# Kernel optimization log

Measured on AMD Instinct MI355X. Metric: run time of the kernel, lower is better.

The kernel has to match this reference:

```python
import jax, jax.numpy as jnp
import numpy as np

NR, NS, TAU, GW = 32, 64, 0.1, 0.5
NEG = jnp.float32(-1e30)

def _nrm(x):
    return x / jnp.maximum(jnp.linalg.norm(x, axis=-1, keepdims=True), 1e-12)

def _pair_loss(fb, ub, am, nm, ra, rp, rn):
    # fb [HW,D] features, ub [HW] uncertainty, am/nm [HW] bool anchor(=pos)/neg masks,
    # ra/rp/rn [HW] uniform random scores standing in for torch.randperm.
    def sel(mask, r, k):  # random subset of size k from mask (invalid slots flagged)
        _, idx = jax.lax.top_k(jnp.where(mask, r, NEG), k)
        return idx, mask[idx]
    def hard(mask, r):  # randperm[:2*Ns] then topk Ns by uncertainty
        cidx, cval = sel(mask, r, 2 * NS)
        _, t = jax.lax.top_k(jnp.where(cval, ub[cidx], NEG), NS)
        return cidx[t], cval[t]
    aidx, aval = sel(am, ra, NR)
    pidx, pval = hard(am, rp)
    nidx, nval = hard(nm, rn)
    q  = _nrm(fb[aidx])   # [NR,D]
    P  = _nrm(fb[pidx])   # [NS,D]
    Ng = _nrm(fb[nidx])   # [NS,D]
    pw = pval.astype(fb.dtype)[:, None]
    nw = nval.astype(fb.dtype)[:, None]
    p = (jnp.exp(P @ q.T / TAU) * pw).sum(0)   # [NR]
    n = (jnp.exp(Ng @ q.T / TAU) * nw).sum(0)  # [NR]
    inc = (am.sum() >= 1) & (nm.sum() >= 1)
    p = p + (1.0 - inc.astype(p.dtype))  # safe when excluded
    per = -jnp.log(p / (p + n + 1e-8))
    af = aval.astype(per.dtype)
    bl = (per * af).sum() / jnp.maximum(af.sum(), 1.0)
    return jnp.where(inc, bl, 0.0), inc

def _forward(feat, labels, prob_ori, prob_aug, unc, r_anc, r_pos, r_neg,
             w1, b1, gamma, beta, w2, b2):
    B, D, H, W = feat.shape
    # proj: 1x1 conv -> BN (training stats) -> relu -> 1x1 conv
    x = jnp.einsum('bdhw,ed->behw', feat, w1) + b1[None, :, None, None]
    mu = x.mean((0, 2, 3), keepdims=True)
    var = x.var((0, 2, 3), keepdims=True)
    x = gamma[None, :, None, None] * (x - mu) / jnp.sqrt(var + 1e-5) + beta[None, :, None, None]
    x = jax.nn.relu(x)
    proj = jnp.einsum('bdhw,ed->behw', x, w2) + b2[None, :, None, None]

    rel = prob_ori.argmax(1) == prob_aug.argmax(1)
    diff = unc > 0.5
    valid = (rel & diff).reshape(B, -1)
    lab = labels.reshape(B, -1)
    f = proj.transpose(0, 2, 3, 1).reshape(B, -1, D)
    uf = unc.reshape(B, -1)
    m1 = valid & (lab == 1)
    m0 = valid & (lab == 0)

    # ---- local loss: classes (1 vs 0) and (0 vs 1) ----
    anc = jnp.stack([m1, m0], 1)  # [B,2,HW]
    neg = jnp.stack([m0, m1], 1)
    pair = jax.vmap(jax.vmap(_pair_loss, in_axes=(None, None, 0, 0, 0, 0, 0)),
                    in_axes=(0, 0, 0, 0, 0, 0, 0))
    bl, inc = pair(f, uf, anc, neg, r_anc, r_pos, r_neg)
    l_local = bl.sum() / jnp.maximum(inc.sum(), 1)

    # ---- global loss with sequential memory bank (bank starts empty) ----
    fgf = m1.astype(f.dtype); bgf = m0.astype(f.dtype)
    cf = fgf.sum(1); cb = bgf.sum(1)
    m_fg = (f * fgf[..., None]).sum(1) / jnp.maximum(cf, 1.0)[:, None]
    m_bg = (f * bgf[..., None]).sum(1) / jnp.maximum(cb, 1.0)[:, None]
    vg = (cf >= 1) & (cb >= 1)
    qf, qb = _nrm(m_fg), _nrm(m_bg)
    # bank content at step b: prototypes of valid j <= b (detached)
    M = ((jnp.arange(B)[None, :] <= jnp.arange(B)[:, None]) & vg[None, :]).astype(f.dtype)  # [b,j]
    Sf = jnp.exp(jax.lax.stop_gradient(qb) @ qf.T / TAU)  # [j,b]
    Sb = jnp.exp(jax.lax.stop_gradient(qf) @ qb.T / TAU)
    nf = jnp.einsum('jb,bj->b', Sf, M)
    nb = jnp.einsum('jb,bj->b', Sb, M)
    pf = jnp.exp((qf * qf).sum(-1) / TAU)
    pb = jnp.exp((qb * qb).sum(-1) / TAU)
    lg = -jnp.log(pf / (pf + nf + 1e-8)) - jnp.log(pb / (pb + nb + 1e-8))
    l_global = (vg.astype(f.dtype) * lg).sum() / jnp.maximum(vg.sum(), 1)

    return l_local + GW * l_global, l_local, l_global

def setup_inputs() -> dict:
    key = jax.random.key(0)
    ks = jax.random.split(key, 16)
    B, D, H, W = 4, 256, 128, 128
    HW = H * W
    return {
        'feat': jax.random.normal(ks[0], (B, D, H, W), jnp.float32),
        'labels': jax.random.randint(ks[1], (B, H, W), 0, 2, jnp.int32),
        'prob_ori': jax.random.uniform(ks[2], (B, 2, H, W), jnp.float32),
        'prob_aug': jax.random.uniform(ks[3], (B, 2, H, W), jnp.float32),
        'unc': jax.random.uniform(ks[4], (B, H, W), jnp.float32),
        'r_anc': jax.random.uniform(ks[5], (B, 2, HW), jnp.float32),
        'r_pos': jax.random.uniform(ks[6], (B, 2, HW), jnp.float32),
        'r_neg': jax.random.uniform(ks[7], (B, 2, HW), jnp.float32),
        'w1': jax.random.normal(ks[8], (D, D), jnp.float32) * 0.05,
        'b1': jnp.zeros((D,), jnp.float32),
        'gamma': jnp.ones((D,), jnp.float32),
        'beta': jnp.zeros((D,), jnp.float32),
        'w2': jax.random.normal(ks[9], (D, D), jnp.float32) * 0.05,
        'b2': jnp.zeros((D,), jnp.float32),
    }

def reference(feat, labels, prob_ori, prob_aug, unc, r_anc, r_pos, r_neg,
              w1, b1, gamma, beta, w2, b2):
    return _forward(feat, labels, prob_ori, prob_aug, unc, r_anc, r_pos, r_neg,
                    w1, b1, gamma, beta, w2, b2)
```

## Files before the change

### kernel.cpp

```cpp
#include <hip/hip_runtime.h>
#include <hip/hip_bf16.h>
#include <float.h>
#include <math.h>

#define HW 16384
#define NBATCH 4
#define DIM 256
#define NEGV (-1e30f)
#define NPP 160

#define OFF_CHAN_SUM 0
#define OFF_CHAN_SQ  1024
#define OFF_MEAN     2048
#define OFF_ISTD     3072
#define OFF_S1       4096
#define OFF_S0       8192
#define OFF_CF       12288
#define OFF_CB       12304
#define OFF_BL       12320
#define OFF_INCF     12352
#define OFF_PPCNT    12416
#define OFF_QBUF     16384
#define OFF_BCNT     24576
#define OFF_MCLS     40960
#define OFF_SELIDX   303104
#define OFF_SELW     308224
#define OFF_ROWS     313344
#define OFF_W1T      1624064
#define OFF_RAW      1886208
#define OFF_CKEYS_XL 68995072
#define WS_NEED_FAST 68995072ull
#define WS_NEED_XL   72140800ull

#define NSEL 24

__device__ __forceinline__ unsigned f2mono(float f) {
  unsigned u = __float_as_uint(f);
  return (u & 0x80000000u) ? ~u : (u | 0x80000000u);
}

__device__ __forceinline__ void sort_desc(unsigned long long* sk, int* si, int n, int tid) {
  for (int ksz = 2; ksz <= n; ksz <<= 1) {
    for (int j = ksz >> 1; j > 0; j >>= 1) {
      __syncthreads();
      if (tid < n) {
        int ixj = tid ^ j;
        if (ixj > tid) {
          unsigned long long a = sk[tid], b = sk[ixj];
          bool up = (tid & ksz) == 0;
          if (up ? (a < b) : (a > b)) {
            sk[tid] = b; sk[ixj] = a;
            int t2 = si[tid]; si[tid] = si[ixj]; si[ixj] = t2;
          }
        }
      }
    }
  }
  __syncthreads();
}

__global__ __launch_bounds__(256) void k_maskc2(
    const float* __restrict__ po, const float* __restrict__ pa,
    const float* __restrict__ unc, const int* __restrict__ lab,
    const float* __restrict__ r_anc, const float* __restrict__ r_pos,
    const float* __restrict__ r_neg, const float* __restrict__ w1,
    int* __restrict__ mcls, int* __restrict__ bcnt,
    unsigned long long* __restrict__ ckeys, float* __restrict__ w1T,
    float* __restrict__ chanSum, float* __restrict__ chanSq,
    float* __restrict__ S1, float* __restrict__ S0,
    int* __restrict__ ppcnt) {
  __shared__ int lcnt[24];
  int tid = threadIdx.x;
  int g = blockIdx.x * 256 + tid;
  int b = g >> 14;
  int lb = blockIdx.x & 63;
  int i = g & (HW - 1);
  if (tid < 24) lcnt[tid] = 0;
  __syncthreads();
  float o0 = po[(size_t)(b*2+0)*HW + i];
  float o1 = po[(size_t)(b*2+1)*HW + i];
  float a0 = pa[(size_t)(b*2+0)*HW + i];
  float a1 = pa[(size_t)(b*2+1)*HW + i];
  bool rel = ((o1 > o0) == (a1 > a0));
  bool valid = rel && (unc[g] > 0.5f);
  int l = lab[g];
  int cls = valid ? ((l == 1) ? 1 : 2) : 0;
  mcls[g] = cls;
  int t0 = 0, t1 = 0, t2 = 0, loc0 = 0, loc1 = 0, loc2 = 0;
  unsigned long long k0 = 0, k1 = 0, k2 = 0;
  if (cls) {
    int co = cls - 1;
    unsigned idxf = (unsigned)(16383 - i);
    t0 = (b*2 + co)*3 + 0;
    t1 = (b*2 + co)*3 + 1;
    t2 = (b*2 + (1 - co))*3 + 2;
    k0 = ((unsigned long long)f2mono(r_anc[(size_t)(b*2 + co)*HW + i]) << 14) | idxf;
    k1 = ((unsigned long long)f2mono(r_pos[(size_t)(b*2 + co)*HW + i]) << 14) | idxf;
    k2 = ((unsigned long long)f2mono(r_neg[(size_t)(b*2 + (1 - co))*HW + i]) << 14) | idxf;
    loc0 = atomicAdd(&lcnt[t0], 1);
    loc1 = atomicAdd(&lcnt[t1], 1);
    loc2 = atomicAdd(&lcnt[t2], 1);
  }
  __syncthreads();
  if (tid < 24 && (tid / 6) == b)
    bcnt[tid*64 + lb] = lcnt[tid];
  if (cls) {
    ckeys[(size_t)t0*HW + lb*256 + loc0] = k0;
    ckeys[(size_t)t1*HW + lb*256 + loc1] = k1;
    ckeys[(size_t)t2*HW + lb*256 + loc2] = k2;
  }
  if (blockIdx.x < 16) {
    int d0 = blockIdx.x * 16;
    float v[16];
    #pragma unroll
    for (int j = 0; j < 16; ++j) v[j] = w1[(size_t)tid*DIM + d0 + j];
    #pragma unroll
    for (int j = 0; j < 16; ++j) w1T[(size_t)(d0 + j)*DIM + tid] = v[j];
  }
  if (blockIdx.x == 16) { chanSum[tid] = 0.f; chanSq[tid] = 0.f; }
  if (blockIdx.x == 17) {
    #pragma unroll
    for (int j = 0; j < 4; ++j) S1[j*256 + tid] = 0.f;
  }
  if (blockIdx.x == 18) {
    #pragma unroll
    for (int j = 0; j < 4; ++j) S0[j*256 + tid] = 0.f;
  }
  if (blockIdx.x == 19 && tid == 0) *ppcnt = 0;
}

__device__ void selc_body(const int* __restrict__ bcnt,
                          const unsigned long long* __restrict__ ckeys,
                          const float* __restrict__ unc,
                          int* __restrict__ selIdx, float* __restrict__ selW,
                          int* __restrict__ cf, int* __restrict__ cb,
                          int task, int tid, char* sh) {
  unsigned long long* sk = (unsigned long long*)sh;
  int* si    = (int*)(sh + 1024);
  int* cIdx  = (int*)(sh + 1536);
  int* hist  = (int*)(sh + 2048);
  int* sufs  = (int*)(sh + 3072);
  int* sbcnt = (int*)(sh + 4096);
  unsigned char* cVal = (unsigned char*)(sh + 4352);
  int* scal  = (int*)(sh + 4480);

  int pair = task / 3, which = task % 3;
  int b = pair >> 1, c = pair & 1;
  const unsigned long long* keys = ckeys + (size_t)task * HW;
  if (tid < 64) sbcnt[tid] = bcnt[task*64 + tid];
  __syncthreads();
  if (tid == 0) { int s = 0; for (int i2 = 0; i2 < 64; ++i2) s += sbcnt[i2]; scal[3] = s; }
  __syncthreads();
  int cnt = scal[3];
  if (which == 0 && tid == 0) { if (c == 0) cf[b] = cnt; else cb[b] = cnt; }
  int K1 = (which == 0) ? 32 : 128;
  int outBase = pair*NPP + (which == 0 ? 0 : (which == 1 ? 32 : 96));

  int mseg = tid >> 2;
  int msub = tid & 3;
  int mcnt = sbcnt[mseg];
  const unsigned long long* mkeys = keys + mseg*256;

  unsigned long long pref = 0;
  if (cnt > K1) {
    const int shifts[6]  = {38, 30, 22, 14, 6, 0};
    const int bitsArr[6] = { 8,  8,  8,  8, 8, 6};
    int k = K1;
    for (int p = 0; p < 6; ++p) {
      int shift = shifts[p], nbits = bitsArr[p], nb = 1 << nbits;
      hist[tid] = 0;
      __syncthreads();
      for (int pos = msub; pos < mcnt; pos += 4) {
        unsigned long long key = mkeys[pos];
        if ((key >> (shift + nbits)) == pref)
          atomicAdd(&hist[(int)((key >> shift) & (nb - 1))], 1);
      }
      __syncthreads();
      if (tid < nb) sufs[tid] = hist[tid];
      __syncthreads();
      for (int off = 1; off < nb; off <<= 1) {
        int add = 0;
        if (tid < nb && tid + off < nb) add = sufs[tid + off];
        __syncthreads();
        if (tid < nb) sufs[tid] += add;
        __syncthreads();
      }
      if (tid < nb) {
        int sthis = sufs[tid];
        int snext = (tid + 1 < nb) ? sufs[tid + 1] : 0;
        if (sthis >= k && snext < k) { scal[0] = tid; scal[1] = k - snext; }
      }
      __syncthreads();
      pref = (pref << nbits) | (unsigned)scal[0];
      k = scal[1];
      __syncthreads();
    }
  }

  if (tid == 0) scal[2] = 0;
  __syncthreads();
  for (int pos = msub; pos < mcnt; pos += 4) {
    unsigned long long key = mkeys[pos];
    if (key >= pref) {
      int p2 = atomicAdd(&scal[2], 1);
      if (p2 < 128) { sk[p2] = key; si[p2] = 16383 - (int)(key & 16383); }
    }
  }
  __syncthreads();
  int gcnt = scal[2];
  if (tid < K1 && tid >= gcnt) { sk[tid] = 0ull; si[tid] = 0; }

  sort_desc(sk, si, K1, tid);

  if (which == 0) {
    if (tid < 32) {
      selIdx[outBase + tid] = si[tid];
      selW[outBase + tid]   = (sk[tid] != 0ull) ? 1.f : 0.f;
    }
    return;
  }

  if (tid < 128) {
    cIdx[tid] = si[tid];
    cVal[tid] = (sk[tid] != 0ull) ? 1 : 0;
  }
  __syncthreads();
  if (tid < 128) {
    float u2 = cVal[tid] ? unc[(size_t)b*HW + cIdx[tid]] : NEGV;
    sk[tid] = ((unsigned long long)f2mono(u2) << 7) | (unsigned)(127 - tid);
    si[tid] = tid;
  }
  sort_desc(sk, si, 128, tid);
  if (tid < 64) {
    int t = si[tid];
    selIdx[outBase + tid] = cIdx[t];
    selW[outBase + tid]   = cVal[t] ? 1.f : 0.f;
  }
}

__global__ __launch_bounds__(256) void k_selc2(
    const int* __restrict__ bcnt, const unsigned long long* __restrict__ ckeys,
    const float* __restrict__ unc,
    int* __restrict__ selIdx, float* __restrict__ selW,
    int* __restrict__ cf, int* __restrict__ cb) {
  __shared__ __align__(16) char sh[4608];
  selc_body(bcnt, ckeys, unc, selIdx, selW, cf, cb, blockIdx.x, threadIdx.x, sh);
}

#define BK 32
#define LDA 128

__device__ void mm8_body(
    const float* __restrict__ feat, const float* __restrict__ w1T,
    const int* __restrict__ mcls,
    float* __restrict__ chanSum, float* __restrict__ chanSq,
    float* __restrict__ rawout, int bid, int tid, float* smem) {
  float* As = smem;
  float* Bs = smem + BK*LDA;
  int ct = bid & 1;
  int rt = bid >> 1;
  int b  = rt >> 7;
  int i0 = (rt & 127) << 7;
  int c0 = ct << 7;
  int tx = tid & 15, ty = tid >> 4;
  float acc[8][8];
  #pragma unroll
  for (int r = 0; r < 8; ++r)
    #pragma unroll
    for (int c = 0; c < 8; ++c) acc[r][c] = 0.f;

  for (int kc = 0; kc < 8; ++kc) {
    int d0 = kc * BK;
    #pragma unroll
    for (int it = 0; it < 4; ++it) {
      int e = it*1024 + tid*4;
      int k = e >> 7, r = e & 127;
      float4 v = *(const float4*)&feat[((size_t)(b*DIM + d0 + k))*HW + i0 + r];
      *(float4*)&As[k*LDA + r] = v;
    }
    #pragma unroll
    for (int it = 0; it < 4; ++it) {
      int e = it*1024 + tid*4;
      int k = e >> 7, c = e & 127;
      float4 v = *(const float4*)&w1T[(size_t)(d0 + k)*DIM + c0 + c];
      *(float4*)&Bs[k*LDA + c] = v;
    }
    __syncthreads();
    #pragma unroll
    for (int k = 0; k < BK; ++k) {
      float4 a0 = *(const float4*)&As[k*LDA + ty*4];
      float4 a1 = *(const float4*)&As[k*LDA + 64 + ty*4];
      float4 b0 = *(const float4*)&Bs[k*LDA + tx*4];
      float4 b1 = *(const float4*)&Bs[k*LDA + 64 + tx*4];
      float ar[8] = {a0.x,a0.y,a0.z,a0.w, a1.x,a1.y,a1.z,a1.w};
      float bc[8] = {b0.x,b0.y,b0.z,b0.w, b1.x,b1.y,b1.z,b1.w};
      #pragma unroll
      for (int r = 0; r < 8; ++r)
        #pragma unroll
        for (int c = 0; c < 8; ++c)
          acc[r][c] += ar[r]*bc[c];
    }
    __syncthreads();
  }

  float* pS = smem;
  float* pQ = smem + 2048;
  #pragma unroll
  for (int c = 0; c < 8; ++c) {
    int lcol = (c < 4) ? (tx*4 + c) : (64 + tx*4 + (c - 4));
    float s = 0.f, q = 0.f;
    #pragma unroll
    for (int r = 0; r < 8; ++r) { float v = acc[r][c]; s += v; q += v*v; }
    pS[ty*128 + lcol] = s;
    pQ[ty*128 + lcol] = q;
  }
  __syncthreads();
  if (tid < 128) {
    float s = 0.f, q = 0.f;
    #pragma unroll
    for (int t2 = 0; t2 < 16; ++t2) { s += pS[t2*128 + tid]; q += pQ[t2*128 + tid]; }
    atomicAdd(&chanSum[c0 + tid], s);
    atomicAdd(&chanSq[c0 + tid],  q);
  }

  #pragma unroll
  for (int r = 0; r < 8; ++r) {
    int lrow = (r < 4) ? (ty*4 + r) : (64 + ty*4 + (r - 4));
    int g = rt*128 + lrow;
    if (mcls[g] != 0) {
      float4 lo; lo.x = acc[r][0]; lo.y = acc[r][1]; lo.z = acc[r][2]; lo.w = acc[r][3];
      float4 hi; hi.x = acc[r][4]; hi.y = acc[r][5]; hi.z = acc[r][6]; hi.w = acc[r][7];
      *(float4*)&rawout[(size_t)g*DIM + c0 + tx*4]      = lo;
      *(float4*)&rawout[(size_t)g*DIM + c0 + 64 + tx*4] = hi;
    }
  }
}

__global__ __launch_bounds__(256) void k_mmsel(
    const float* __restrict__ feat, const float* __restrict__ w1T,
    const int* __restrict__ mcls,
    float* __restrict__ chanSum, float* __restrict__ chanSq,
    float* __restrict__ rawout,
    const int* __restrict__ bcnt, const unsigned long long* __restrict__ ckeys,
    const float* __restrict__ unc,
    int* __restrict__ selIdx, float* __restrict__ selW,
    int* __restrict__ cf, int* __restrict__ cb, int nSel) {
  __shared__ __align__(16) float smem[2*BK*LDA];
  int bid = blockIdx.x;
  if (bid < nSel)
    selc_body(bcnt, ckeys, unc, selIdx, selW, cf, cb, bid, threadIdx.x, (char*)smem);
  else
    mm8_body(feat, w1T, mcls, chanSum, chanSq, rawout, bid - nSel, threadIdx.x, smem);
}

__global__ __launch_bounds__(256) void k_post(
    const float* __restrict__ raw, const int* __restrict__ mcls,
    const float* __restrict__ chanSum, const float* __restrict__ chanSq,
    const float* __restrict__ gamma, const float* __restrict__ beta,
    const float* __restrict__ w2, const float* __restrict__ b2,
    const int* __restrict__ selIdx, const float* __restrict__ selW,
    float* __restrict__ S1, float* __restrict__ S0,
    float* __restrict__ rows) {
  __shared__ __align__(16) float sh[2048];
  const float nconst = (float)(NBATCH * HW);
  int tid = threadIdx.x;

  if (blockIdx.x < 256) {
    float* p1 = sh;
    float* p2 = sh + 1024;
    int w = tid >> 6, lane = tid & 63;
    int p0 = blockIdx.x << 8;
    int b = p0 >> 14;
    int ch = lane*4;
    float4 G = *(const float4*)&gamma[ch];
    float4 Bt = *(const float4*)&beta[ch];
    float4 CS = *(const float4*)&chanSum[ch];
    float4 CQ = *(const float4*)&chanSq[ch];
    float m0 = CS.x/nconst, m1 = CS.y/nconst, m2 = CS.z/nconst, m3 = CS.w/nconst;
    float v0 = CQ.x/nconst - m0*m0, v1 = CQ.y/nconst - m1*m1;
    float v2 = CQ.z/nconst - m2*m2, v3 = CQ.w/nconst - m3*m3;
    float i0 = 1.0f/sqrtf(v0 + 1e-5f), i1 = 1.0f/sqrtf(v1 + 1e-5f);
    float i2 = 1.0f/sqrtf(v2 + 1e-5f), i3 = 1.0f/sqrtf(v3 + 1e-5f);
    float A0 = G.x*i0, A1 = G.y*i1, A2 = G.z*i2, A3 = G.w*i3;
    float s1[4] = {0,0,0,0}, s0[4] = {0,0,0,0};
    int g0 = p0 + w*64;
    for (int t = 0; t < 64; ++t) {
      int g = g0 + t;
      int cls = mcls[g];
      if (cls == 0) continue;
      float4 v = *(const float4*)&raw[(size_t)g*DIM + ch];
      float r0 = A0*(v.x - m0) + Bt.x; r0 = r0 > 0.f ? r0 : 0.f;
      float r1 = A1*(v.y - m1) + Bt.y; r1 = r1 > 0.f ? r1 : 0.f;
      float r2 = A2*(v.z - m2) + Bt.z; r2 = r2 > 0.f ? r2 : 0.f;
      float r3 = A3*(v.w - m3) + Bt.w; r3 = r3 > 0.f ? r3 : 0.f;
      if (cls == 1) { s1[0]+=r0; s1[1]+=r1; s1[2]+=r2; s1[3]+=r3; }
      else          { s0[0]+=r0; s0[1]+=r1; s0[2]+=r2; s0[3]+=r3; }
    }
    #pragma unroll
    for (int j = 0; j < 4; ++j) {
      p1[w*256 + ch + j] = s1[j];
      p2[w*256 + ch + j] = s0[j];
    }
    __syncthreads();
    float a = p1[tid] + p1[256+tid] + p1[512+tid] + p1[768+tid];
    float d = p2[tid] + p2[256+tid] + p2[512+tid] + p2[768+tid];
    atomicAdd(&S1[b*DIM + tid], a);
    atomicAdd(&S0[b*DIM + tid], d);
  } else {
    float* rl  = sh;
    float* red = sh + 1024;
    int blk = blockIdx.x - 256;
    int slot0 = blk * 4;
    int pair = slot0 / NPP;
    int b = pair >> 1;
    int e = tid;
    float m = chanSum[e] / nconst;
    float v = chanSq[e] / nconst - m*m;
    float istd = 1.0f / sqrtf(v + 1e-5f);
    float A = gamma[e]*istd;
    float Bt = beta[e];
    bool ok[4];
    #pragma unroll
    for (int s = 0; s < 4; ++s) {
      int slot = slot0 + s;
      ok[s] = (selW[slot] != 0.f);
      float rv = 0.f;
      if (ok[s]) {
        int i = selIdx[slot];
        float acc = raw[((size_t)b*HW + i)*DIM + e];
        float bn = A*(acc - m) + Bt;
        rv = bn > 0.f ? bn : 0.f;
      }
      rl[s*256 + e] = rv;
    }
    __syncthreads();
    float b2e = b2[e];
    float pj[4] = {b2e, b2e, b2e, b2e};
    const float4* w4 = (const float4*)&w2[(size_t)e*DIM];
    #pragma unroll 8
    for (int d4 = 0; d4 < DIM/4; ++d4) {
      float4 w = w4[d4];
      #pragma unroll
      for (int s = 0; s < 4; ++s) {
        float4 a = *(const float4*)&rl[s*256 + d4*4];
        pj[s] += a.x*w.x + a.y*w.y + a.z*w.z + a.w*w.w;
      }
    }
    #pragma unroll
    for (int s = 0; s < 4; ++s) red[s*256 + e] = pj[s]*pj[s];
    __syncthreads();
    for (int off = 128; off > 0; off >>= 1) {
      if (e < off) {
        #pragma unroll
        for (int s = 0; s < 4; ++s) red[s*256 + e] += red[s*256 + e + off];
      }
      __syncthreads();
    }
    #pragma unroll
    for (int s = 0; s < 4; ++s) {
      float sc = 1.f / fmaxf(sqrtf(red[s*256]), 1e-12f);
      rows[(size_t)(slot0 + s)*DIM + e] = ok[s] ? pj[s]*sc : 0.f;
    }
  }
}

__device__ void pair_body(
    const float* __restrict__ rows, const float* __restrict__ selW,
    const int* __restrict__ cf, const int* __restrict__ cb,
    float* __restrict__ BL, float* __restrict__ INCF, int pair, int tid) {
  __shared__ float q[32*257];
  __shared__ float pacc[256], nacc[256];
  __shared__ float red[64];
  int b = pair >> 1, c = pair & 1;
  for (int l = tid; l < 32*DIM; l += 256) {
    int r = l >> 8, d = l & 255;
    q[r*257 + d] = rows[((size_t)pair*NPP + r)*DIM + d];
  }
  __syncthreads();
  int g = tid >> 5, r = tid & 31;
  float ap = 0.f, an = 0.f;
  for (int so = 0; so < 8; ++so) {
    int s = so*8 + g;
    const float* Pr = &rows[((size_t)pair*NPP + 32 + s)*DIM];
    const float* Nr = &rows[((size_t)pair*NPP + 96 + s)*DIM];
    float dp = 0.f, dn = 0.f;
    for (int d = 0; d < DIM; ++d) {
      float qv = q[r*257 + d];
      dp += Pr[d]*qv;
      dn += Nr[d]*qv;
    }
    ap += expf(dp*10.f) * selW[pair*NPP + 32 + s];
    an += expf(dn*10.f) * selW[pair*NPP + 96 + s];
  }
  pacc[tid] = ap; nacc[tid] = an;
  __syncthreads();
  if (tid < 32) {
    float p = 0.f, n = 0.f;
    for (int gg = 0; gg < 8; ++gg) { p += pacc[gg*32 + tid]; n += nacc[gg*32 + tid]; }
    int amC = (c == 0) ? cf[b] : cb[b];
    int nmC = (c == 0) ? cb[b] : cf[b];
    bool inc = (amC >= 1) && (nmC >= 1);
    if (!inc) p += 1.f;
    float per = -logf(p / (p + n + 1e-8f));
    float af = selW[pair*NPP + tid];
    red[tid]      = per*af;
    red[32 + tid] = af;
  }
  __syncthreads();
  if (tid == 0) {
    float s = 0.f, sa = 0.f;
    for (int rr = 0; rr < 32; ++rr) { s += red[rr]; sa += red[32+rr]; }
    int amC = (c == 0) ? cf[b] : cb[b];
    int nmC = (c == 0) ? cb[b] : cf[b];
    bool inc = (amC >= 1) && (nmC >= 1);
    float bl = s / fmaxf(sa, 1.f);
    BL[pair]   = inc ? bl : 0.f;
    INCF[pair] = inc ? 1.f : 0.f;
  }
}

__device__ void proto_body(
    const float* __restrict__ S1, const float* __restrict__ S0,
    const int* __restrict__ cf, const int* __restrict__ cb,
    const float* __restrict__ w2, const float* __restrict__ b2,
    float* __restrict__ qbuf, int idx, int l) {
  int b = idx >> 1, side = idx & 1;
  const float* S = (side == 0) ? &S1[b*DIM] : &S0[b*DIM];
  float cnt = (float)((side == 0) ? cf[b] : cb[b]);
  float m[4]; float n2p = 0.f;
  #pragma unroll
  for (int k = 0; k < 4; ++k) {
    int e = l + 64*k;
    float acc = 0.f;
    const float* w2r = &w2[(size_t)e*DIM];
    for (int d = 0; d < DIM; ++d) acc += S[d]*w2r[d];
    float mv = (acc + cnt*b2[e]) / fmaxf(cnt, 1.f);
    m[k] = mv; n2p += mv*mv;
  }
  #pragma unroll
  for (int off = 32; off > 0; off >>= 1) n2p += __shfl_down(n2p, off, 64);
  float n2 = __shfl(n2p, 0, 64);
  float sc = 1.f / fmaxf(sqrtf(n2), 1e-12f);
  #pragma unroll
  for (int k = 0; k < 4; ++k)
    qbuf[(size_t)(side*4 + b)*DIM + l + 64*k] = m[k]*sc;
}

__device__ void glob_body(
    const float* __restrict__ qbuf,
    const int* __restrict__ cf, const int* __restrict__ cb,
    const float* __restrict__ BL, const float* __restrict__ INCF,
    float* __restrict__ out, int l) {
  float qf[4][4], qb[4][4];
  #pragma unroll
  for (int b = 0; b < 4; ++b)
    #pragma unroll
    for (int k = 0; k < 4; ++k) {
      qf[b][k] = qbuf[(size_t)b*DIM + l + 64*k];
      qb[b][k] = qbuf[(size_t)(4 + b)*DIM + l + 64*k];
    }
  float pd[24];
  #pragma unroll
  for (int j = 0; j < 4; ++j)
    #pragma unroll
    for (int b = 0; b < 4; ++b) {
      float s = 0.f;
      #pragma unroll
      for (int k = 0; k < 4; ++k) s += qb[j][k]*qf[b][k];
      pd[j*4 + b] = s;
    }
  #pragma unroll
  for (int b = 0; b < 4; ++b) {
    float s1 = 0.f, s2 = 0.f;
    #pragma unroll
    for (int k = 0; k < 4; ++k) { s1 += qf[b][k]*qf[b][k]; s2 += qb[b][k]*qb[b][k]; }
    pd[16 + b] = s1; pd[20 + b] = s2;
  }
  #pragma unroll
  for (int t = 0; t < 24; ++t)
    #pragma unroll
    for (int off = 32; off > 0; off >>= 1)
      pd[t] += __shfl_down(pd[t], off, 64);
  if (l == 0) {
    bool vg[4]; float vgs = 0.f;
    for (int b = 0; b < 4; ++b) {
      vg[b] = (cf[b] >= 1) && (cb[b] >= 1);
      if (vg[b]) vgs += 1.f;
    }
    float gsum = 0.f;
    for (int b = 0; b < 4; ++b) {
      float nf = 0.f, nb = 0.f;
      for (int j = 0; j <= b; ++j) if (vg[j]) {
        nf += expf(10.f*pd[j*4 + b]);
        nb += expf(10.f*pd[b*4 + j]);
      }
      float pf = expf(10.f*pd[16 + b]);
      float pb = expf(10.f*pd[20 + b]);
      float lg = -logf(pf/(pf + nf + 1e-8f)) - logf(pb/(pb + nb + 1e-8f));
      if (vg[b]) gsum += lg;
    }
    float l_global = gsum / fmaxf(vgs, 1.f);
    float bls = 0.f, incs = 0.f;
    for (int p = 0; p < 8; ++p) { bls += BL[p]; incs += INCF[p]; }
    float l_local = bls / fmaxf(incs, 1.f);
    out[0] = l_local + 0.5f*l_global;
    out[1] = l_local;
    out[2] = l_global;
  }
}

__global__ __launch_bounds__(256) void k_pp(
    const float* __restrict__ rows, const float* __restrict__ selW,
    const int* __restrict__ cf, const int* __restrict__ cb,
    float* __restrict__ BL, float* __restrict__ INCF,
    const float* __restrict__ S1, const float* __restrict__ S0,
    const float* __restrict__ w2, const float* __restrict__ b2,
    float* __restrict__ qbuf, int* __restrict__ ppcnt,
    float* __restrict__ out) {
  __shared__ int isLast;
  if (blockIdx.x < 8) {
    pair_body(rows, selW, cf, cb, BL, INCF, blockIdx.x, threadIdx.x);
  } else {
    if (threadIdx.x < 64)
      proto_body(S1, S0, cf, cb, w2, b2, qbuf, blockIdx.x - 8, threadIdx.x);
  }
  __syncthreads();
  __threadfence();
  if (threadIdx.x == 0) isLast = (atomicAdd(ppcnt, 1) == 15);
  __syncthreads();
  if (isLast) {
    __threadfence();
    if (threadIdx.x < 64)
      glob_body(qbuf, cf, cb, BL, INCF, out, threadIdx.x);
  }
}

__global__ void k_mask(const float* __restrict__ po, const float* __restrict__ pa,
                       const float* __restrict__ unc, const int* __restrict__ lab,
                       int* __restrict__ mcls, int* __restrict__ cf, int* __restrict__ cb) {
  int g = blockIdx.x * 256 + threadIdx.x;
  int b = g >> 14;
  int i = g & (HW - 1);
  float o0 = po[(size_t)(b*2+0)*HW + i];
  float o1 = po[(size_t)(b*2+1)*HW + i];
  float a0 = pa[(size_t)(b*2+0)*HW + i];
  float a1 = pa[(size_t)(b*2+1)*HW + i];
  bool rel = ((o1 > o0) == (a1 > a0));
  bool valid = rel && (unc[g] > 0.5f);
  int l = lab[g];
  int cls = valid ? ((l == 1) ? 1 : 2) : 0;
  mcls[g] = cls;
  if (cls == 1) atomicAdd(&cf[b], 1);
  if (cls == 2) atomicAdd(&cb[b], 1);
}

template<int MODE>
__global__ __launch_bounds__(256) void k_matmul(
    const float* __restrict__ feat, const float* __restrict__ w1,
    float* __restrict__ chanSum, float* __restrict__ chanSq,
    const float* __restrict__ meanr, const float* __restrict__ istd,
    const float* __restrict__ gamma, const float* __restrict__ beta,
    const int* __restrict__ mcls,
    float* __restrict__ S1, float* __restrict__ S0) {
  __shared__ __align__(16) float As[64*68];
  __shared__ __align__(16) float Bs[64*68];
  __shared__ float cA[64], cB[64];
  int tid = threadIdx.x;
  int rt = blockIdx.x;
  int ct = blockIdx.y;
  int b  = rt >> 8;
  int i0 = (rt & 255) << 6;
  int c0 = ct << 6;
  int tx = tid & 15, ty = tid >> 4;
  float acc[4][4] = {{0.f,0.f,0.f,0.f},{0.f,0.f,0.f,0.f},{0.f,0.f,0.f,0.f},{0.f,0.f,0.f,0.f}};
  for (int kc = 0; kc < 4; ++kc) {
    int d0 = kc << 6;
    #pragma unroll
    for (int it = 0; it < 4; ++it) {
      int k  = it*16 + (tid >> 4);
      int rq = tid & 15;
      float4 v = *(const float4*)&feat[((size_t)(b*DIM + d0 + k))*HW + i0 + rq*4];
      *(float4*)&As[k*68 + rq*4] = v;
    }
    #pragma unroll
    for (int it = 0; it < 4; ++it) {
      int col = it*16 + (tid >> 4);
      int kq  = tid & 15;
      float4 v = *(const float4*)&w1[(size_t)(c0 + col)*DIM + d0 + kq*4];
      Bs[(kq*4+0)*68 + col] = v.x;
      Bs[(kq*4+1)*68 + col] = v.y;
      Bs[(kq*4+2)*68 + col] = v.z;
      Bs[(kq*4+3)*68 + col] = v.w;
    }
    __syncthreads();
    #pragma unroll
    for (int k = 0; k < 64; ++k) {
      float4 av = *(const float4*)&As[k*68 + ty*4];
      float4 bv = *(const float4*)&Bs[k*68 + tx*4];
      float aa[4] = {av.x, av.y, av.z, av.w};
      float bb[4] = {bv.x, bv.y, bv.z, bv.w};
      #pragma unroll
      for (int rr = 0; rr < 4; ++rr)
        #pragma unroll
        for (int cc = 0; cc < 4; ++cc)
          acc[rr][cc] += aa[rr]*bb[cc];
    }
    __syncthreads();
  }
  if (tid < 64) { cA[tid] = 0.f; cB[tid] = 0.f; }
  __syncthreads();
  if (MODE == 0) {
    float s[4] = {0,0,0,0}, q[4] = {0,0,0,0};
    #pragma unroll
    for (int rr = 0; rr < 4; ++rr)
      #pragma unroll
      for (int cc = 0; cc < 4; ++cc) { float v = acc[rr][cc]; s[cc] += v; q[cc] += v*v; }
    #pragma unroll
    for (int cc = 0; cc < 4; ++cc) {
      atomicAdd(&cA[tx*4+cc], s[cc]);
      atomicAdd(&cB[tx*4+cc], q[cc]);
    }
    __syncthreads();
    if (tid < 64) {
      atomicAdd(&chanSum[c0 + tid], cA[tid]);
      atomicAdd(&chanSq[c0 + tid],  cB[tid]);
    }
  } else {
    float A[4], M[4], Bt[4];
    #pragma unroll
    for (int cc = 0; cc < 4; ++cc) {
      int c = c0 + tx*4 + cc;
      A[cc] = gamma[c]*istd[c]; M[cc] = meanr[c]; Bt[cc] = beta[c];
    }
    float s1[4] = {0,0,0,0}, s0[4] = {0,0,0,0};
    #pragma unroll
    for (int rr = 0; rr < 4; ++rr) {
      int g = rt*64 + ty*4 + rr;
      int cls = mcls[g];
      if (cls == 0) continue;
      #pragma unroll
      for (int cc = 0; cc < 4; ++cc) {
        float v = A[cc]*(acc[rr][cc] - M[cc]) + Bt[cc];
        v = v > 0.f ? v : 0.f;
        if (cls == 1) s1[cc] += v; else s0[cc] += v;
      }
    }
    #pragma unroll
    for (int cc = 0; cc < 4; ++cc) {
      atomicAdd(&cA[tx*4+cc], s1[cc]);
      atomicAdd(&cB[tx*4+cc], s0[cc]);
    }
    __syncthreads();
    if (tid < 64) {
      atomicAdd(&S1[b*DIM + c0 + tid], cA[tid]);
      atomicAdd(&S0[b*DIM + c0 + tid], cB[tid]);
    }
  }
}

__global__ void k_stats(const float* __restrict__ chanSum, const float* __restrict__ chanSq,
                        float* __restrict__ meanr, float* __restrict__ istd) {
  int e = threadIdx.x;
  const float n = (float)(NBATCH * HW);
  float m = chanSum[e] / n;
  float v = chanSq[e] / n - m*m;
  meanr[e] = m;
  istd[e]  = 1.0f / sqrtf(v + 1e-5f);
}

__global__ __launch_bounds__(256) void k_select(
    const int* __restrict__ mcls,
    const float* __restrict__ r_anc, const float* __restrict__ r_pos, const float* __restrict__ r_neg,
    const float* __restrict__ unc,
    int* __restrict__ selIdx, float* __restrict__ selW) {
  __shared__ int hist[256];
  __shared__ int sufs[256];
  __shared__ unsigned long long sk[128];
  __shared__ int si[128];
  __shared__ int cIdx[128];
  __shared__ unsigned char cVal[128];
  __shared__ int sh_bin, sh_k, gcnt;

  int tid  = threadIdx.x;
  int task = blockIdx.x;
  int pair = task / 3, which = task % 3;
  int b = pair >> 1, c = pair & 1;
  int wantA = (c == 0) ? 1 : 2;
  int want  = (which == 2) ? (3 - wantA) : wantA;
  const int* mc = mcls + (size_t)b * HW;
  const float* r = (which == 0) ? r_anc : (which == 1 ? r_pos : r_neg);
  r += (size_t)(b*2 + c) * HW;

  int K1 = (which == 0) ? 32 : 128;
  int outBase = pair*NPP + (which == 0 ? 0 : (which == 1 ? 32 : 96));

  const int shifts[6]  = {38, 30, 22, 14, 6, 0};
  const int bitsArr[6] = { 8,  8,  8,  8, 8, 6};
  unsigned long long pref = 0;
  int k = K1;
  for (int p = 0; p < 6; ++p) {
    int shift = shifts[p];
    int nbits = bitsArr[p];
    int nb = 1 << nbits;
    hist[tid] = 0;
    __syncthreads();
    int lastBin = -1, lc = 0;
    #pragma unroll 4
    for (int j = 0; j < 64; ++j) {
      int i = tid + j*256;
      float kv = (mc[i] == want) ? r[i] : NEGV;
      unsigned long long key = ((unsigned long long)f2mono(kv) << 14) | (unsigned)(16383 - i);
      if ((key >> (shift + nbits)) == pref) {
        int bin = (int)((key >> shift) & (nb - 1));
        if (bin == lastBin) { ++lc; }
        else {
          if (lastBin >= 0) atomicAdd(&hist[lastBin], lc);
          lastBin = bin; lc = 1;
        }
      }
    }
    if (lastBin >= 0) atomicAdd(&hist[lastBin], lc);
    __syncthreads();
    if (tid < nb) sufs[tid] = hist[tid];
    __syncthreads();
    for (int off = 1; off < nb; off <<= 1) {
      int add = 0;
      if (tid < nb && tid + off < nb) add = sufs[tid + off];
      __syncthreads();
      if (tid < nb) sufs[tid] += add;
      __syncthreads();
    }
    if (tid < nb) {
      int sthis = sufs[tid];
      int snext = (tid + 1 < nb) ? sufs[tid + 1] : 0;
      if (sthis >= k && snext < k) { sh_bin = tid; sh_k = k - snext; }
    }
    __syncthreads();
    pref = (pref << nbits) | (unsigned)sh_bin;
    k = sh_k;
    __syncthreads();
  }

  if (tid == 0) gcnt = 0;
  __syncthreads();
  #pragma unroll 4
  for (int j = 0; j < 64; ++j) {
    int i = tid + j*256;
    float kv = (mc[i] == want) ? r[i] : NEGV;
    unsigned long long key = ((unsigned long long)f2mono(kv) << 14) | (unsigned)(16383 - i);
    if (key >= pref) {
      int p2 = atomicAdd(&gcnt, 1);
      if (p2 < 128) { sk[p2] = key; si[p2] = i; }
    }
  }
  __syncthreads();
  if (tid < K1 && tid >= gcnt) { sk[tid] = 0ull; si[tid] = 0; }

  sort_desc(sk, si, K1, tid);

  if (which == 0) {
    if (tid < 32) {
      selIdx[outBase + tid] = si[tid];
      selW[outBase + tid]   = ((sk[tid] >> 14) >= 0x80000000ull) ? 1.f : 0.f;
    }
    return;
  }

  if (tid < 128) {
    cIdx[tid] = si[tid];
    cVal[tid] = ((sk[tid] >> 14) >= 0x80000000ull) ? 1 : 0;
  }
  __syncthreads();
  if (tid < 128) {
    float u2 = cVal[tid] ? unc[(size_t)b*HW + cIdx[tid]] : NEGV;
    sk[tid] = ((unsigned long long)f2mono(u2) << 7) | (unsigned)(127 - tid);
    si[tid] = tid;
  }
  sort_desc(sk, si, 128, tid);
  if (tid < 64) {
    int t = si[tid];
    selIdx[outBase + tid] = cIdx[t];
    selW[outBase + tid]   = cVal[t] ? 1.f : 0.f;
  }
}

__global__ __launch_bounds__(256) void k_rowproj(
    const float* __restrict__ feat, const float* __restrict__ w1, const float* __restrict__ w2,
    const float* __restrict__ b2, const float* __restrict__ gamma, const float* __restrict__ beta,
    const float* __restrict__ meanr, const float* __restrict__ istd,
    const int* __restrict__ selIdx, float* __restrict__ rows) {
  __shared__ __align__(16) float fr[DIM];
  __shared__ __align__(16) float rl[DIM];
  __shared__ float red[256];
  int slot = blockIdx.x;
  int pair = slot / NPP;
  int b = pair >> 1;
  int i = selIdx[slot];
  int e = threadIdx.x;
  fr[e] = feat[((size_t)(b*DIM + e))*HW + i];
  __syncthreads();
  float acc = 0.f;
  {
    const float4* f4 = (const float4*)fr;
    const float4* w4 = (const float4*)&w1[(size_t)e*DIM];
    #pragma unroll 8
    for (int d = 0; d < DIM/4; ++d) {
      float4 a = f4[d], w = w4[d];
      acc += a.x*w.x + a.y*w.y + a.z*w.z + a.w*w.w;
    }
  }
  float bn = gamma[e]*istd[e]*(acc - meanr[e]) + beta[e];
  rl[e] = bn > 0.f ? bn : 0.f;
  __syncthreads();
  float pj = b2[e];
  {
    const float4* f4 = (const float4*)rl;
    const float4* w4 = (const float4*)&w2[(size_t)e*DIM];
    #pragma unroll 8
    for (int d = 0; d < DIM/4; ++d) {
      float4 a = f4[d], w = w4[d];
      pj += a.x*w.x + a.y*w.y + a.z*w.z + a.w*w.w;
    }
  }
  red[e] = pj*pj;
  __syncthreads();
  for (int off = 128; off > 0; off >>= 1) {
    if (e < off) red[e] += red[e+off];
    __syncthreads();
  }
  float sc = 1.f / fmaxf(sqrtf(red[0]), 1e-12f);
  rows[(size_t)slot*DIM + e] = pj * sc;
}

__global__ __launch_bounds__(256) void k_pair(
    const float* __restrict__ rows, const float* __restrict__ selW,
    const int* __restrict__ cf, const int* __restrict__ cb,
    float* __restrict__ BL, float* __restrict__ INCF) {
  pair_body(rows, selW, cf, cb, BL, INCF, blockIdx.x, threadIdx.x);
}

__global__ __launch_bounds__(64) void k_proto(
    const float* __restrict__ S1, const float* __restrict__ S0,
    const int* __restrict__ cf, const int* __restrict__ cb,
    const float* __restrict__ w2, const float* __restrict__ b2,
    float* __restrict__ qbuf) {
  proto_body(S1, S0, cf, cb, w2, b2, qbuf, blockIdx.x, threadIdx.x);
}

__global__ __launch_bounds__(64) void k_glob(
    const float* __restrict__ qbuf,
    const int* __restrict__ cf, const int* __restrict__ cb,
    const float* __restrict__ BL, const float* __restrict__ INCF,
    float* __restrict__ out) {
  glob_body(qbuf, cf, cb, BL, INCF, out, threadIdx.x);
}

extern "C" void kernel_launch(void* const* d_in, const int* in_sizes, int n_in,
                              void* d_out, int out_size, void* d_ws, size_t ws_size,
                              hipStream_t stream) {
  const float* feat     = (const float*)d_in[0];
  const int*   labels   = (const int*)  d_in[1];
  const float* prob_ori = (const float*)d_in[2];
  const float* prob_aug = (const float*)d_in[3];
  const float* unc      = (const float*)d_in[4];
  const float* r_anc    = (const float*)d_in[5];
  const float* r_pos    = (const float*)d_in[6];
  const float* r_neg    = (const float*)d_in[7];
  const float* w1       = (const float*)d_in[8];
  const float* gamma    = (const float*)d_in[10];
  const float* beta     = (const float*)d_in[11];
  const float* w2       = (const float*)d_in[12];
  const float* b2       = (const float*)d_in[13];

  char* ws = (char*)d_ws;
  float* chanSum = (float*)(ws + OFF_CHAN_SUM);
  float* chanSq  = (float*)(ws + OFF_CHAN_SQ);
  float* meanr   = (float*)(ws + OFF_MEAN);
  float* istd    = (float*)(ws + OFF_ISTD);
  float* S1      = (float*)(ws + OFF_S1);
  float* S0      = (float*)(ws + OFF_S0);
  int*   cf      = (int*)  (ws + OFF_CF);
  int*   cb      = (int*)  (ws + OFF_CB);
  float* BLp     = (float*)(ws + OFF_BL);
  float* INCp    = (float*)(ws + OFF_INCF);
  int*   ppcnt   = (int*)  (ws + OFF_PPCNT);
  float* qbuf    = (float*)(ws + OFF_QBUF);
  int*   bcnt    = (int*)  (ws + OFF_BCNT);
  int*   mclsp   = (int*)  (ws + OFF_MCLS);
  int*   selIdx  = (int*)  (ws + OFF_SELIDX);
  float* selW    = (float*)(ws + OFF_SELW);
  float* rowsbuf = (float*)(ws + OFF_ROWS);
  float* w1T     = (float*)(ws + OFF_W1T);
  float* rawbuf  = (float*)(ws + OFF_RAW);

  if (ws_size >= WS_NEED_FAST) {
    bool xl = (ws_size >= WS_NEED_XL);
    unsigned long long* ckeys = (unsigned long long*)(ws + (xl ? OFF_CKEYS_XL : OFF_RAW));

    k_maskc2<<<256, 256, 0, stream>>>(prob_ori, prob_aug, unc, labels,
                                      r_anc, r_pos, r_neg, w1,
                                      mclsp, bcnt, ckeys, w1T,
                                      chanSum, chanSq, S1, S0, ppcnt);
    if (xl) {
      k_mmsel<<<1024 + NSEL, 256, 0, stream>>>(feat, w1T, mclsp, chanSum, chanSq, rawbuf,
                                               bcnt, ckeys, unc, selIdx, selW, cf, cb, NSEL);
    } else {
      k_selc2<<<24, 256, 0, stream>>>(bcnt, ckeys, unc, selIdx, selW, cf, cb);
      k_mmsel<<<1024, 256, 0, stream>>>(feat, w1T, mclsp, chanSum, chanSq, rawbuf,
                                        bcnt, ckeys, unc, selIdx, selW, cf, cb, 0);
    }

    k_post<<<576, 256, 0, stream>>>(rawbuf, mclsp, chanSum, chanSq, gamma, beta,
                                    w2, b2, selIdx, selW, S1, S0, rowsbuf);

    k_pp<<<16, 256, 0, stream>>>(rowsbuf, selW, cf, cb, BLp, INCp,
                                 S1, S0, w2, b2, qbuf, ppcnt, (float*)d_out);
  } else {
    hipMemsetAsync(d_ws, 0, 16384, stream);
    k_mask<<<256, 256, 0, stream>>>(prob_ori, prob_aug, unc, labels, mclsp, cf, cb);
    dim3 gmm(1024, 4);
    k_matmul<0><<<gmm, 256, 0, stream>>>(feat, w1, chanSum, chanSq,
                                         meanr, istd, gamma, beta, mclsp, S1, S0);
    k_stats<<<1, 256, 0, stream>>>(chanSum, chanSq, meanr, istd);
    k_matmul<1><<<gmm, 256, 0, stream>>>(feat, w1, chanSum, chanSq,
                                         meanr, istd, gamma, beta, mclsp, S1, S0);
    k_select<<<24, 256, 0, stream>>>(mclsp, r_anc, r_pos, r_neg, unc, selIdx, selW);
    k_rowproj<<<1280, 256, 0, stream>>>(feat, w1, w2, b2, gamma, beta, meanr, istd,
                                        selIdx, rowsbuf);
    k_pair<<<8, 256, 0, stream>>>(rowsbuf, selW, cf, cb, BLp, INCp);
    k_proto<<<8, 64, 0, stream>>>(S1, S0, cf, cb, w2, b2, qbuf);
    k_glob<<<1, 64, 0, stream>>>(qbuf, cf, cb, BLp, INCp, (float*)d_out);
  }
}
```

Baseline: 299.5 us.

## Unroll masked class-sum loads and split row projection to one slot per block

The class-sum branch of k_post now batches four mask reads and their conditional float4 loads before computing, so more memory loads are in flight at once. The row-projection branch goes from four selected slots per block to one, and the launch grows from 576 to 1536 blocks so the 1280 projection slots are spread across more workgroups. The cost is that each w2 row is re-read once per slot instead of once per four slots, and there are more blocks with their own reduction overhead.

```diff
diff --git a/kernel.cpp b/kernel.cpp
--- a/kernel.cpp
+++ b/kernel.cpp
@@ -384,17 +384,27 @@
     float A0 = G.x*i0, A1 = G.y*i1, A2 = G.z*i2, A3 = G.w*i3;
     float s1[4] = {0,0,0,0}, s0[4] = {0,0,0,0};
     int g0 = p0 + w*64;
-    for (int t = 0; t < 64; ++t) {
-      int g = g0 + t;
-      int cls = mcls[g];
-      if (cls == 0) continue;
-      float4 v = *(const float4*)&raw[(size_t)g*DIM + ch];
-      float r0 = A0*(v.x - m0) + Bt.x; r0 = r0 > 0.f ? r0 : 0.f;
-      float r1 = A1*(v.y - m1) + Bt.y; r1 = r1 > 0.f ? r1 : 0.f;
-      float r2 = A2*(v.z - m2) + Bt.z; r2 = r2 > 0.f ? r2 : 0.f;
-      float r3 = A3*(v.w - m3) + Bt.w; r3 = r3 > 0.f ? r3 : 0.f;
-      if (cls == 1) { s1[0]+=r0; s1[1]+=r1; s1[2]+=r2; s1[3]+=r3; }
-      else          { s0[0]+=r0; s0[1]+=r1; s0[2]+=r2; s0[3]+=r3; }
+    for (int t = 0; t < 64; t += 4) {
+      int cls4[4];
+      float4 v4[4];
+      #pragma unroll
+      for (int j = 0; j < 4; ++j) { v4[j].x = v4[j].y = v4[j].z = v4[j].w = 0.f; }
+      #pragma unroll
+      for (int j = 0; j < 4; ++j) cls4[j] = mcls[g0 + t + j];
+      #pragma unroll
+      for (int j = 0; j < 4; ++j)
+        if (cls4[j]) v4[j] = *(const float4*)&raw[(size_t)(g0 + t + j)*DIM + ch];
+      #pragma unroll
+      for (int j = 0; j < 4; ++j) {
+        if (cls4[j] == 0) continue;
+        float4 v = v4[j];
+        float r0 = A0*(v.x - m0) + Bt.x; r0 = r0 > 0.f ? r0 : 0.f;
+        float r1 = A1*(v.y - m1) + Bt.y; r1 = r1 > 0.f ? r1 : 0.f;
+        float r2 = A2*(v.z - m2) + Bt.z; r2 = r2 > 0.f ? r2 : 0.f;
+        float r3 = A3*(v.w - m3) + Bt.w; r3 = r3 > 0.f ? r3 : 0.f;
+        if (cls4[j] == 1) { s1[0]+=r0; s1[1]+=r1; s1[2]+=r2; s1[3]+=r3; }
+        else              { s0[0]+=r0; s0[1]+=r1; s0[2]+=r2; s0[3]+=r3; }
+      }
     }
     #pragma unroll
     for (int j = 0; j < 4; ++j) {
@@ -409,9 +419,8 @@
   } else {
     float* rl  = sh;
     float* red = sh + 1024;
-    int blk = blockIdx.x - 256;
-    int slot0 = blk * 4;
-    int pair = slot0 / NPP;
+    int slot = blockIdx.x - 256;
+    int pair = slot / NPP;
     int b = pair >> 1;
     int e = tid;
     float m = chanSum[e] / nconst;
@@ -419,48 +428,32 @@
     float istd = 1.0f / sqrtf(v + 1e-5f);
     float A = gamma[e]*istd;
     float Bt = beta[e];
-    bool ok[4];
-    #pragma unroll
-    for (int s = 0; s < 4; ++s) {
-      int slot = slot0 + s;
-      ok[s] = (selW[slot] != 0.f);
-      float rv = 0.f;
-      if (ok[s]) {
-        int i = selIdx[slot];
-        float acc = raw[((size_t)b*HW + i)*DIM + e];
-        float bn = A*(acc - m) + Bt;
-        rv = bn > 0.f ? bn : 0.f;
-      }
-      rl[s*256 + e] = rv;
-    }
-    __syncthreads();
-    float b2e = b2[e];
-    float pj[4] = {b2e, b2e, b2e, b2e};
+    bool ok = (selW[slot] != 0.f);
+    float rv = 0.f;
+    if (ok) {
+      int i = selIdx[slot];
+      float acc = raw[((size_t)b*HW + i)*DIM + e];
+      float bn = A*(acc - m) + Bt;
+      rv = bn > 0.f ? bn : 0.f;
+    }
+    rl[e] = rv;
+    __syncthreads();
+    float pj = b2[e];
     const float4* w4 = (const float4*)&w2[(size_t)e*DIM];
     #pragma unroll 8
     for (int d4 = 0; d4 < DIM/4; ++d4) {
       float4 w = w4[d4];
-      #pragma unroll
-      for (int s = 0; s < 4; ++s) {
-        float4 a = *(const float4*)&rl[s*256 + d4*4];
-        pj[s] += a.x*w.x + a.y*w.y + a.z*w.z + a.w*w.w;
-      }
-    }
-    #pragma unroll
-    for (int s = 0; s < 4; ++s) red[s*256 + e] = pj[s]*pj[s];
+      float4 a = *(const float4*)&rl[d4*4];
+      pj += a.x*w.x + a.y*w.y + a.z*w.z + a.w*w.w;
+    }
+    red[e] = pj*pj;
     __syncthreads();
     for (int off = 128; off > 0; off >>= 1) {
-      if (e < off) {
-        #pragma unroll
-        for (int s = 0; s < 4; ++s) red[s*256 + e] += red[s*256 + e + off];
-      }
+      if (e < off) red[e] += red[e+off];
       __syncthreads();
     }
-    #pragma unroll
-    for (int s = 0; s < 4; ++s) {
-      float sc = 1.f / fmaxf(sqrtf(red[s*256]), 1e-12f);
-      rows[(size_t)(slot0 + s)*DIM + e] = ok[s] ? pj[s]*sc : 0.f;
-    }
+    float sc = 1.f / fmaxf(sqrtf(red[0]), 1e-12f);
+    rows[(size_t)slot*DIM + e] = ok ? pj*sc : 0.f;
   }
 }
 
@@ -1010,8 +1003,8 @@
                                         bcnt, ckeys, unc, selIdx, selW, cf, cb, 0);
     }
 
-    k_post<<<576, 256, 0, stream>>>(rawbuf, mclsp, chanSum, chanSq, gamma, beta,
-                                    w2, b2, selIdx, selW, S1, S0, rowsbuf);
+    k_post<<<1536, 256, 0, stream>>>(rawbuf, mclsp, chanSum, chanSq, gamma, beta,
+                                     w2, b2, selIdx, selW, S1, S0, rowsbuf);
 
     k_pp<<<16, 256, 0, stream>>>(rowsbuf, selW, cf, cb, BLp, INCp,
                                  S1, S0, w2, b2, qbuf, ppcnt, (float*)d_out);
```

Result: no change. 302.7 us (median of 2 runs) (+1.1%).
